# Performance work log

Hardware: AMD Instinct MI355X
Metric: run time of the kernel (lower is better)

Reference implementation:

```python
import jax, jax.numpy as jnp
import numpy as np


def setup_inputs() -> dict:
    key = jax.random.key(0)
    ks = jax.random.split(key, 7)
    B, T, E, H = 256, 512, 256, 256
    s = 1.0 / np.sqrt(E + H)
    return {
        "embedding": jax.random.normal(ks[0], (B, T, E), dtype=jnp.float32),
        "Wz": jax.random.normal(ks[1], (H, E + H), dtype=jnp.float32) * s,
        "bz": jax.random.normal(ks[2], (H,), dtype=jnp.float32) * s,
        "Wr": jax.random.normal(ks[3], (H, E + H), dtype=jnp.float32) * s,
        "br": jax.random.normal(ks[4], (H,), dtype=jnp.float32) * s,
        "Wm": jax.random.normal(ks[5], (H, E + H), dtype=jnp.float32) * s,
        "bm": jax.random.normal(ks[6], (H,), dtype=jnp.float32) * s,
    }


def reference(embedding, Wz, bz, Wr, br, Wm, bm):
    # embedding: [B, T, E] -> time-major [T, B, E] (matches Encoder.forward transpose)
    emb = jnp.transpose(embedding, (1, 0, 2))
    B = emb.shape[1]
    H = Wz.shape[0]
    h0 = jnp.zeros((B, H), dtype=embedding.dtype)

    def step(h, x):  # x: [B, E], h: [B, H]
        xi = jnp.concatenate([x, h], axis=1)            # [B, E+H]
        z = jax.nn.sigmoid(xi @ Wz.T + bz)              # update gate
        r = jax.nn.sigmoid(xi @ Wr.T + br)              # reset gate
        xm = jnp.concatenate([x, r * h], axis=1)
        h_cand = jnp.tanh(xm @ Wm.T + bm)
        h_new = (1.0 - z) * h + z * h_cand
        return h_new, h_new

    _, hs = jax.lax.scan(step, h0, emb)                 # hs: [T, B, H]
    return jnp.transpose(hs, (1, 0, 2))                 # [B, T, H]
```

## Files before the change

kernel.cpp:

```cpp
#include <hip/hip_runtime.h>

typedef _Float16 half8_t __attribute__((ext_vector_type(8)));
typedef _Float16 half2_t __attribute__((ext_vector_type(2)));
typedef float floatx4 __attribute__((ext_vector_type(4)));

#define B_DIM 256
#define T_DIM 512
#define E_DIM 256
#define H_DIM 256
#define MROWS (B_DIM * T_DIM)

__device__ __forceinline__ half2_t mk2(_Float16 x, _Float16 y) {
    half2_t v; v[0] = x; v[1] = y; return v;
}

__global__ __launch_bounds__(256, 2) void gemm_x(
    const float* __restrict__ emb,
    const float* __restrict__ Wz, const float* __restrict__ bz,
    const float* __restrict__ Wr, const float* __restrict__ br,
    const float* __restrict__ Wm, const float* __restrict__ bm,
    _Float16* __restrict__ Xz, _Float16* __restrict__ Xr,
    float* __restrict__ Xm)
{
    const int n0 = blockIdx.x * 128;
    const int m0 = blockIdx.y * 128;
    const int gate = n0 >> 8;
    const int ng0 = n0 & 255;
    const float* W    = (gate == 0) ? Wz : (gate == 1) ? Wr : Wm;
    const float* bias = (gate == 0) ? bz : (gate == 1) ? br : bm;

    __shared__ __align__(16) _Float16 lA[128 * 40];
    __shared__ __align__(16) _Float16 lB[128 * 40];

    const int t = threadIdx.x;
    const int lane = t & 63;
    const int wave = t >> 6;
    const int wm = (wave >> 1) * 64;
    const int wn = (wave & 1) * 64;
    const int lq = lane >> 4;
    const int lr = lane & 15;

    floatx4 acc[4][4];
    #pragma unroll
    for (int i = 0; i < 4; ++i)
        #pragma unroll
        for (int j = 0; j < 4; ++j)
            acc[i][j] = (floatx4)0.0f;

    const int srow = t >> 1;
    const int scol = (t & 1) * 16;
    const float* aSrc = emb + (size_t)(m0 + srow) * E_DIM + scol;
    const float* bSrc = W + (size_t)(ng0 + srow) * (E_DIM + H_DIM) + scol;

    for (int k0 = 0; k0 < E_DIM; k0 += 32) {
        float ta[16], tb[16];
        #pragma unroll
        for (int u = 0; u < 4; ++u) {
            *(float4*)(ta + 4 * u) = *(const float4*)(aSrc + k0 + 4 * u);
            *(float4*)(tb + 4 * u) = *(const float4*)(bSrc + k0 + 4 * u);
        }
        half8_t a0, a1, b0, b1;
        #pragma unroll
        for (int u = 0; u < 8; ++u) {
            a0[u] = (_Float16)ta[u]; a1[u] = (_Float16)ta[u + 8];
            b0[u] = (_Float16)tb[u]; b1[u] = (_Float16)tb[u + 8];
        }
        __syncthreads();
        *(half8_t*)&lA[srow * 40 + scol]     = a0;
        *(half8_t*)&lA[srow * 40 + scol + 8] = a1;
        *(half8_t*)&lB[srow * 40 + scol]     = b0;
        *(half8_t*)&lB[srow * 40 + scol + 8] = b1;
        __syncthreads();

        half8_t af[4], bf[4];
        #pragma unroll
        for (int i = 0; i < 4; ++i)
            af[i] = *(const half8_t*)&lA[(wm + i * 16 + lr) * 40 + lq * 8];
        #pragma unroll
        for (int j = 0; j < 4; ++j)
            bf[j] = *(const half8_t*)&lB[(wn + j * 16 + lr) * 40 + lq * 8];
        #pragma unroll
        for (int i = 0; i < 4; ++i)
            #pragma unroll
            for (int j = 0; j < 4; ++j)
                acc[i][j] = __builtin_amdgcn_mfma_f32_16x16x32_f16(
                    af[i], bf[j], acc[i][j], 0, 0, 0);
    }

    if (gate < 2) {
        _Float16* dst = (gate == 0) ? Xz : Xr;
        #pragma unroll
        for (int j = 0; j < 4; ++j) {
            const int ng = ng0 + wn + j * 16 + lr;
            const float bv = bias[ng];
            #pragma unroll
            for (int i = 0; i < 4; ++i) {
                const int mrow = m0 + wm + i * 16 + lq * 4;
                #pragma unroll
                for (int r = 0; r < 4; ++r)
                    dst[(size_t)(mrow + r) * H_DIM + ng] =
                        (_Float16)(acc[i][j][r] + bv);
            }
        }
    } else {
        #pragma unroll
        for (int j = 0; j < 4; ++j) {
            const int ng = ng0 + wn + j * 16 + lr;
            const float bv = bias[ng];
            #pragma unroll
            for (int i = 0; i < 4; ++i) {
                const int mrow = m0 + wm + i * 16 + lq * 4;
                #pragma unroll
                for (int r = 0; r < 4; ++r)
                    Xm[(size_t)(mrow + r) * H_DIM + ng] = acc[i][j][r] + bv;
            }
        }
    }
}

__device__ __forceinline__ float pick4(floatx4 v, int r) {
    float x01 = (r & 1) ? v[1] : v[0];
    float x23 = (r & 1) ? v[3] : v[2];
    return (r & 2) ? x23 : x01;
}

__global__ __launch_bounds__(512, 2) void gru_rec(
    const float* __restrict__ Wz,
    const float* __restrict__ Wr,
    const float* __restrict__ Wm,
    const _Float16* __restrict__ Xz,
    const _Float16* __restrict__ Xr,
    float* __restrict__ out)
{
    const int b = blockIdx.x;
    const int t = threadIdx.x;
    const int w    = t >> 6;
    const int lane = t & 63;
    const int lr   = lane & 15;
    const int lq   = lane >> 4;

    __shared__ __align__(16) _Float16 hh[256];
    __shared__ __align__(16) float    hf[256];
    __shared__ __align__(16) _Float16 rh[256];
    __shared__ __align__(16) float    zl[256];

    half8_t af[4][8];
    {
        const float* Wg = (w < 4) ? Wz : Wr;
        #pragma unroll
        for (int i = 0; i < 4; ++i) {
            const float* rp = Wg +
                (size_t)(((w & 3) * 4 + i) * 16 + lr) * (E_DIM + H_DIM) +
                E_DIM + lq * 8;
            #pragma unroll
            for (int kt = 0; kt < 8; ++kt) {
                float4 f0 = *(const float4*)(rp + kt * 32);
                float4 f1 = *(const float4*)(rp + kt * 32 + 4);
                half8_t hv;
                hv[0] = (_Float16)f0.x; hv[1] = (_Float16)f0.y;
                hv[2] = (_Float16)f0.z; hv[3] = (_Float16)f0.w;
                hv[4] = (_Float16)f1.x; hv[5] = (_Float16)f1.y;
                hv[6] = (_Float16)f1.z; hv[7] = (_Float16)f1.w;
                af[i][kt] = hv;
            }
        }
    }
    half8_t am[2][8];
    {
        #pragma unroll
        for (int i = 0; i < 2; ++i) {
            const float* rp = Wm +
                (size_t)((w * 2 + i) * 16 + lr) * (E_DIM + H_DIM) +
                E_DIM + lq * 8;
            #pragma unroll
            for (int kt = 0; kt < 8; ++kt) {
                float4 f0 = *(const float4*)(rp + kt * 32);
                float4 f1 = *(const float4*)(rp + kt * 32 + 4);
                half8_t hv;
                hv[0] = (_Float16)f0.x; hv[1] = (_Float16)f0.y;
                hv[2] = (_Float16)f0.z; hv[3] = (_Float16)f0.w;
                hv[4] = (_Float16)f1.x; hv[5] = (_Float16)f1.y;
                hv[6] = (_Float16)f1.z; hv[7] = (_Float16)f1.w;
                am[i][kt] = hv;
            }
        }
    }

    if (t < 256) { hh[t] = (_Float16)0.0f; hf[t] = 0.0f; }
    __syncthreads();

    const int rowA = (w & 3) * 64 + (lr >> 2) * 16 + lq * 4 + (lr & 3);
    const int row2 = w * 32 + ((lr >> 2) & 1) * 16 + lq * 4 + (lr & 3);

    const size_t rowbase = (size_t)b * T_DIM * H_DIM;
    const _Float16* Xg = (w < 4) ? Xz : Xr;

    _Float16 xg_p = Xg[rowbase + rowA];
    float    xm_p = (lr < 8) ? out[rowbase + row2] : 0.0f;

    for (int ts = 0; ts < T_DIM; ++ts) {
        floatx4 acc[4];
        acc[0] = (floatx4)0.0f; acc[1] = (floatx4)0.0f;
        acc[2] = (floatx4)0.0f; acc[3] = (floatx4)0.0f;
        #pragma unroll
        for (int kt = 0; kt < 8; ++kt) {
            half8_t bf = *(const half8_t*)&hh[kt * 32 + lq * 8];
            #pragma unroll
            for (int i = 0; i < 4; ++i)
                acc[i] = __builtin_amdgcn_mfma_f32_16x16x32_f16(
                    af[i][kt], bf, acc[i], 0, 0, 0);
        }
        {
            const int r = lr & 3;
            float s0 = pick4(acc[0], r), s1 = pick4(acc[1], r);
            float s2 = pick4(acc[2], r), s3 = pick4(acc[3], r);
            float v = (lr & 8) ? ((lr & 4) ? s3 : s2)
                               : ((lr & 4) ? s1 : s0);
            const float a = v + (float)xg_p;
            const float g = 1.0f / (1.0f + __expf(-a));
            if (w < 4) zl[rowA] = g;
            else       rh[rowA] = (_Float16)(g * hf[rowA]);
        }
        if (ts + 1 < T_DIM)
            xg_p = Xg[rowbase + (size_t)(ts + 1) * H_DIM + rowA];
        __syncthreads();

        floatx4 acc2[2];
        acc2[0] = (floatx4)0.0f; acc2[1] = (floatx4)0.0f;
        #pragma unroll
        for (int kt = 0; kt < 8; ++kt) {
            half8_t bfm = *(const half8_t*)&rh[kt * 32 + lq * 8];
            #pragma unroll
            for (int i = 0; i < 2; ++i)
                acc2[i] = __builtin_amdgcn_mfma_f32_16x16x32_f16(
                    am[i][kt], bfm, acc2[i], 0, 0, 0);
        }
        if (lr < 8) {
            const int r = lr & 3;
            float u0 = pick4(acc2[0], r), u1 = pick4(acc2[1], r);
            float v2 = (lr & 4) ? u1 : u0;
            const float amv = v2 + xm_p;
            const float hc  = 2.0f / (1.0f + __expf(-2.0f * amv)) - 1.0f;
            const float z   = zl[row2];
            const float hp  = hf[row2];
            const float hn  = hp + z * (hc - hp);
            out[rowbase + (size_t)ts * H_DIM + row2] = hn;
            hf[row2] = hn;
            hh[row2] = (_Float16)hn;
            if (ts + 1 < T_DIM)
                xm_p = out[rowbase + (size_t)(ts + 1) * H_DIM + row2];
        }
        __syncthreads();
    }
}

extern "C" void kernel_launch(void* const* d_in, const int* in_sizes, int n_in,
                              void* d_out, int out_size, void* d_ws, size_t ws_size,
                              hipStream_t stream) {
    (void)in_sizes; (void)n_in; (void)out_size; (void)ws_size;
    const float* emb = (const float*)d_in[0];
    const float* Wz  = (const float*)d_in[1];
    const float* bz  = (const float*)d_in[2];
    const float* Wr  = (const float*)d_in[3];
    const float* br  = (const float*)d_in[4];
    const float* Wm  = (const float*)d_in[5];
    const float* bm  = (const float*)d_in[6];
    float* out = (float*)d_out;

    _Float16* Xz = (_Float16*)d_ws;
    _Float16* Xr = Xz + (size_t)MROWS * H_DIM;

    dim3 g1(6, MROWS / 128);
    gemm_x<<<g1, 256, 0, stream>>>(emb, Wz, bz, Wr, br, Wm, bm, Xz, Xr, out);
    gru_rec<<<B_DIM, 512, 0, stream>>>(Wz, Wr, Wm, Xz, Xr, out);
}
```

Baseline: 1.019 ms.

## Stage gate inputs in LDS via async DMA and batch hidden-state stores

The recurrent kernel now loads the precomputed Xz, Xr and Xm projections for 8 timesteps at a time into double-buffered LDS, using global_load_lds. The load for the next block is issued during the last step of the current block. New hidden states are collected in an LDS history buffer and written to the output once per 8 steps as coalesced float4 stores, instead of scalar per-step global stores. This is meant to take global memory latency and scattered stores off the serial per-step critical path. The cost is extra LDS and reliance on barriers to order the asynchronous LDS loads.

```diff
diff --git a/kernel.cpp b/kernel.cpp
--- a/kernel.cpp
+++ b/kernel.cpp
@@ -12,6 +12,14 @@
 
 __device__ __forceinline__ half2_t mk2(_Float16 x, _Float16 y) {
     half2_t v; v[0] = x; v[1] = y; return v;
+}
+
+__device__ __forceinline__ void dma1k(const void* g, void* l, int lane) {
+    __builtin_amdgcn_global_load_lds(
+        (const __attribute__((address_space(1))) unsigned int*)
+            ((const char*)g + lane * 16),
+        (__attribute__((address_space(3))) unsigned int*)l,
+        16, 0, 0);
 }
 
 __global__ __launch_bounds__(256, 2) void gemm_x(
@@ -143,6 +151,10 @@
     __shared__ __align__(16) float    hf[256];
     __shared__ __align__(16) _Float16 rh[256];
     __shared__ __align__(16) float    zl[256];
+    __shared__ __align__(16) _Float16 xzS[4096];
+    __shared__ __align__(16) _Float16 xrS[4096];
+    __shared__ __align__(16) float    xmS[4096];
+    __shared__ __align__(16) float    hist[2048];
 
     half8_t af[4][8];
     {
@@ -186,71 +198,94 @@
         }
     }
 
+    const int rowA = (w & 3) * 64 + (lr >> 2) * 16 + lq * 4 + (lr & 3);
+    const int row2 = w * 32 + ((lr >> 2) & 1) * 16 + lq * 4 + (lr & 3);
+
+    const size_t rowbase = (size_t)b * T_DIM * H_DIM;
+    const _Float16* XgS = (w < 4) ? xzS : xrS;
+
+    auto stage_block = [&](int row0, int buf) {
+        const size_t base = rowbase + (size_t)row0 * H_DIM;
+        #pragma unroll
+        for (int qq = 0; qq < 2; ++qq) {
+            const int q = w * 2 + qq;
+            if (q < 4)
+                dma1k(Xz + base + q * 512,
+                      (void*)(xzS + buf * 2048 + q * 512), lane);
+            else if (q < 8)
+                dma1k(Xr + base + (q - 4) * 512,
+                      (void*)(xrS + buf * 2048 + (q - 4) * 512), lane);
+            else
+                dma1k(out + base + (q - 8) * 256,
+                      (void*)(xmS + buf * 2048 + (q - 8) * 256), lane);
+        }
+    };
+
+    stage_block(0, 0);
     if (t < 256) { hh[t] = (_Float16)0.0f; hf[t] = 0.0f; }
     __syncthreads();
 
-    const int rowA = (w & 3) * 64 + (lr >> 2) * 16 + lq * 4 + (lr & 3);
-    const int row2 = w * 32 + ((lr >> 2) & 1) * 16 + lq * 4 + (lr & 3);
-
-    const size_t rowbase = (size_t)b * T_DIM * H_DIM;
-    const _Float16* Xg = (w < 4) ? Xz : Xr;
-
-    _Float16 xg_p = Xg[rowbase + rowA];
-    float    xm_p = (lr < 8) ? out[rowbase + row2] : 0.0f;
-
-    for (int ts = 0; ts < T_DIM; ++ts) {
-        floatx4 acc[4];
-        acc[0] = (floatx4)0.0f; acc[1] = (floatx4)0.0f;
-        acc[2] = (floatx4)0.0f; acc[3] = (floatx4)0.0f;
-        #pragma unroll
-        for (int kt = 0; kt < 8; ++kt) {
-            half8_t bf = *(const half8_t*)&hh[kt * 32 + lq * 8];
-            #pragma unroll
-            for (int i = 0; i < 4; ++i)
-                acc[i] = __builtin_amdgcn_mfma_f32_16x16x32_f16(
-                    af[i][kt], bf, acc[i], 0, 0, 0);
-        }
+    for (int ts8 = 0; ts8 < T_DIM; ts8 += 8) {
+        const int cur = (ts8 >> 3) & 1;
+        #pragma unroll
+        for (int j = 0; j < 8; ++j) {
+            if (j == 7 && ts8 + 8 < T_DIM)
+                stage_block(ts8 + 8, cur ^ 1);
+
+            floatx4 acc[4];
+            acc[0] = (floatx4)0.0f; acc[1] = (floatx4)0.0f;
+            acc[2] = (floatx4)0.0f; acc[3] = (floatx4)0.0f;
+            #pragma unroll
+            for (int kt = 0; kt < 8; ++kt) {
+                half8_t bf = *(const half8_t*)&hh[kt * 32 + lq * 8];
+                #pragma unroll
+                for (int i = 0; i < 4; ++i)
+                    acc[i] = __builtin_amdgcn_mfma_f32_16x16x32_f16(
+                        af[i][kt], bf, acc[i], 0, 0, 0);
+            }
+            {
+                const int r = lr & 3;
+                float s0 = pick4(acc[0], r), s1 = pick4(acc[1], r);
+                float s2 = pick4(acc[2], r), s3 = pick4(acc[3], r);
+                float v = (lr & 8) ? ((lr & 4) ? s3 : s2)
+                                   : ((lr & 4) ? s1 : s0);
+                const float a = v + (float)XgS[cur * 2048 + j * 256 + rowA];
+                const float g = 1.0f / (1.0f + __expf(-a));
+                if (w < 4) zl[rowA] = g;
+                else       rh[rowA] = (_Float16)(g * hf[rowA]);
+            }
+            __syncthreads();
+
+            floatx4 acc2[2];
+            acc2[0] = (floatx4)0.0f; acc2[1] = (floatx4)0.0f;
+            #pragma unroll
+            for (int kt = 0; kt < 8; ++kt) {
+                half8_t bfm = *(const half8_t*)&rh[kt * 32 + lq * 8];
+                #pragma unroll
+                for (int i = 0; i < 2; ++i)
+                    acc2[i] = __builtin_amdgcn_mfma_f32_16x16x32_f16(
+                        am[i][kt], bfm, acc2[i], 0, 0, 0);
+            }
+            if (lr < 8) {
+                const int r = lr & 3;
+                float u0 = pick4(acc2[0], r), u1 = pick4(acc2[1], r);
+                float v2 = (lr & 4) ? u1 : u0;
+                const float amv = v2 + xmS[cur * 2048 + j * 256 + row2];
+                const float hc  = 2.0f / (1.0f + __expf(-2.0f * amv)) - 1.0f;
+                const float z   = zl[row2];
+                const float hp  = hf[row2];
+                const float hn  = hp + z * (hc - hp);
+                hist[j * 256 + row2] = hn;
+                hf[row2] = hn;
+                hh[row2] = (_Float16)hn;
+            }
+            __syncthreads();
+        }
+
         {
-            const int r = lr & 3;
-            float s0 = pick4(acc[0], r), s1 = pick4(acc[1], r);
-            float s2 = pick4(acc[2], r), s3 = pick4(acc[3], r);
-            float v = (lr & 8) ? ((lr & 4) ? s3 : s2)
-                               : ((lr & 4) ? s1 : s0);
-            const float a = v + (float)xg_p;
-            const float g = 1.0f / (1.0f + __expf(-a));
-            if (w < 4) zl[rowA] = g;
-            else       rh[rowA] = (_Float16)(g * hf[rowA]);
-        }
-        if (ts + 1 < T_DIM)
-            xg_p = Xg[rowbase + (size_t)(ts + 1) * H_DIM + rowA];
-        __syncthreads();
-
-        floatx4 acc2[2];
-        acc2[0] = (floatx4)0.0f; acc2[1] = (floatx4)0.0f;
-        #pragma unroll
-        for (int kt = 0; kt < 8; ++kt) {
-            half8_t bfm = *(const half8_t*)&rh[kt * 32 + lq * 8];
-            #pragma unroll
-            for (int i = 0; i < 2; ++i)
-                acc2[i] = __builtin_amdgcn_mfma_f32_16x16x32_f16(
-                    am[i][kt], bfm, acc2[i], 0, 0, 0);
-        }
-        if (lr < 8) {
-            const int r = lr & 3;
-            float u0 = pick4(acc2[0], r), u1 = pick4(acc2[1], r);
-            float v2 = (lr & 4) ? u1 : u0;
-            const float amv = v2 + xm_p;
-            const float hc  = 2.0f / (1.0f + __expf(-2.0f * amv)) - 1.0f;
-            const float z   = zl[row2];
-            const float hp  = hf[row2];
-            const float hn  = hp + z * (hc - hp);
-            out[rowbase + (size_t)ts * H_DIM + row2] = hn;
-            hf[row2] = hn;
-            hh[row2] = (_Float16)hn;
-            if (ts + 1 < T_DIM)
-                xm_p = out[rowbase + (size_t)(ts + 1) * H_DIM + row2];
-        }
-        __syncthreads();
+            const float4 hv4 = *(const float4*)&hist[t * 4];
+            *(float4*)&out[rowbase + (size_t)ts8 * H_DIM + t * 4] = hv4;
+        }
     }
 }
 
```

New measurement: 1.048 ms. +2.8%, slower.
